# Kernel tuning notes

Measured on AMD Instinct MI355X. Metric: run time of the kernel, lower is better.

The kernel has to match this reference:

```python
import jax, jax.numpy as jnp
import numpy as np

HEADS = 8
DIM_HEAD = 64
SCALE = DIM_HEAD ** -0.5
DIM = 128
HIDDEN = HEADS * DIM_HEAD  # 512


def setup_inputs() -> dict:
    key = jax.random.key(0)
    k1, k2, k3 = jax.random.split(key, 3)
    x = jax.random.normal(k1, (1, DIM, 16, 16, 16), jnp.float32)
    # 1x1x1 Conv3d weights are equivalent to dense (out_ch, in_ch) matrices
    w_qkv = jax.random.normal(k2, (3 * HIDDEN, DIM), jnp.float32) * (DIM ** -0.5)
    w_out = jax.random.normal(k3, (DIM, HIDDEN), jnp.float32) * (HIDDEN ** -0.5)
    b_out = jnp.zeros((DIM,), jnp.float32)
    return {"x": x, "w_qkv": w_qkv, "w_out": w_out, "b_out": b_out}


def reference(x, w_qkv, w_out, b_out):
    b, c, D, H, W = x.shape
    n = D * H * W
    # 1x1x1 conv QKV projection, then split channels as (3, heads, dim_head)
    qkv = jnp.einsum('oc,bcdhw->bodhw', w_qkv, x).reshape(b, 3, HEADS, DIM_HEAD, n)
    q, k, v = qkv[:, 0], qkv[:, 1], qkv[:, 2]  # each (b, h, dim_head, n)
    q = q * SCALE
    # full attention over the flattened 3D volume (n = d*h*w tokens)
    sim = jnp.einsum('bhdi,bhdj->bhij', q, k)           # (b, h, n, n)
    attn = jax.nn.softmax(sim, axis=-1)                 # stable softmax (amax subtracted internally)
    out = jnp.einsum('bhij,bhdj->bhid', attn, v)        # (b, h, n, dim_head)
    out = out.transpose(0, 1, 3, 2).reshape(b, HIDDEN, D, H, W)  # b (h d) x y z
    # 1x1x1 output conv with bias
    out = jnp.einsum('oc,bcdhw->bodhw', w_out, out) + b_out[None, :, None, None, None]
    return out
```

## Files before the change

### kernel.cpp

```cpp
#include <hip/hip_runtime.h>
#include <hip/hip_fp16.h>


#define HEADS 8
#define DHEAD 64
#define NPOS 4096
#define CIN 128
#define HID 512
#define QK_SCALE 0.125f
#define NLOG2E 1.4426950408889634f
#define EXP_BIAS 11.541560327111707f

typedef _Float16 f16;
typedef _Float16 f16x8 __attribute__((ext_vector_type(8)));
typedef _Float16 f16x4 __attribute__((ext_vector_type(4)));
typedef float f32x4 __attribute__((ext_vector_type(4)));

__global__ __launch_bounds__(256) void wconv_kernel(const float* __restrict__ wo,
                                                    f16* __restrict__ woh) {
  int i = (blockIdx.x * 256 + threadIdx.x) * 4;
  f32x4 v = *(const f32x4*)&wo[i];
  f16x4 o = {(f16)v.x, (f16)v.y, (f16)v.z, (f16)v.w};
  *(f16x4*)&woh[i] = o;
}

__global__ __launch_bounds__(256) void qkv_kernel(
    const float* __restrict__ x, const float* __restrict__ w,
    f16* __restrict__ QT, f16* __restrict__ KT, f16* __restrict__ V) {
  __shared__ float xs[64][132];
  __shared__ f16 st[64][72];
  const int bid = blockIdx.x;
  const int ot = bid % 24, pt = bid / 24;
  const int o0 = ot * 64, p0 = pt * 64;
  const int t = threadIdx.x;

  for (int idx = t; idx < 64 * 128; idx += 256) {
    int c = idx >> 6, p = idx & 63;
    xs[p][c] = x[c * NPOS + p0 + p];
  }
  __syncthreads();

  const int pl = (t & 15) * 4;
  const int ol = (t >> 4) * 4;
  float acc[4][4] = {};
  const float* wbase = w + o0 * CIN;
#pragma unroll 4
  for (int c = 0; c < CIN; c += 4) {
    f32x4 xv[4], wv[4];
#pragma unroll
    for (int j = 0; j < 4; ++j) xv[j] = *(const f32x4*)&xs[pl + j][c];
#pragma unroll
    for (int i = 0; i < 4; ++i) wv[i] = *(const f32x4*)&wbase[(ol + i) * CIN + c];
#pragma unroll
    for (int i = 0; i < 4; ++i)
#pragma unroll
      for (int j = 0; j < 4; ++j)
        acc[i][j] += wv[i].x * xv[j].x + wv[i].y * xv[j].y +
                     wv[i].z * xv[j].z + wv[i].w * xv[j].w;
  }

  const int region = o0 >> 9;
  const float scl = (region == 0) ? QK_SCALE : 1.0f;
  if (region < 2) {
#pragma unroll
    for (int i = 0; i < 4; ++i)
#pragma unroll
      for (int j = 0; j < 4; ++j)
        st[pl + j][ol + i] = (f16)(acc[i][j] * scl);
  } else {
#pragma unroll
    for (int i = 0; i < 4; ++i)
#pragma unroll
      for (int j = 0; j < 4; ++j)
        st[ol + i][pl + j] = (f16)acc[i][j];
  }
  __syncthreads();

  const int h = (o0 >> 6) & 7;
  const int row = t >> 2, seg = t & 3;
  const uint4* srcp = (const uint4*)&st[row][seg * 16];
  uint4 v0 = srcp[0], v1 = srcp[1];
  f16* dst;
  if (region == 0)      dst = QT + ((size_t)(h * NPOS + p0 + row)) * DHEAD + seg * 16;
  else if (region == 1) dst = KT + ((size_t)(h * NPOS + p0 + row)) * DHEAD + seg * 16;
  else                  dst = V + ((size_t)(h * DHEAD + row)) * NPOS + p0 + seg * 16;
  ((uint4*)dst)[0] = v0;
  ((uint4*)dst)[1] = v1;
}

__global__ __launch_bounds__(256) void attn_kernel(
    const f16* __restrict__ QT, const f16* __restrict__ KT,
    const f16* __restrict__ V, f16* __restrict__ ATf) {
  __shared__ f16 kbuf[2][4096];
  __shared__ f16 vbuf[2][4096];
  __shared__ f16 plds[4][16][72];
  const int bid = blockIdx.x;
  const int h = bid & 7;
  const int i0 = (bid >> 3) * 64;
  const int t = threadIdx.x;
  const int w = t >> 6, l = t & 63;
  const int g = l >> 4, q = l & 15;
  const int qx = q & 7;

  const f16* kbase = KT + (size_t)h * NPOS * DHEAD;
  const f16* vbase = V + (size_t)h * DHEAD * NPOS;

  const int s0 = w * 128 + l, s1 = s0 + 64;
  const int r0 = s0 >> 3, c0 = (s0 & 7) ^ (r0 & 7);
  const int r1 = s1 >> 3, c1 = (s1 & 7) ^ (r1 & 7);
  const f16* kS0 = kbase + r0 * DHEAD + c0 * 8;
  const f16* kS1 = kbase + r1 * DHEAD + c1 * 8;
  const f16* vS0 = vbase + (size_t)r0 * NPOS + c0 * 8;
  const f16* vS1 = vbase + (size_t)r1 * NPOS + c1 * 8;

#define STAGE(b, j0) do {                                                        \
    __builtin_amdgcn_global_load_lds(                                            \
      (const __attribute__((address_space(1))) unsigned int*)(kS0 + (j0) * DHEAD), \
      (__attribute__((address_space(3))) unsigned int*)(&kbuf[b][w * 1024]), 16, 0, 0); \
    __builtin_amdgcn_global_load_lds(                                            \
      (const __attribute__((address_space(1))) unsigned int*)(kS1 + (j0) * DHEAD), \
      (__attribute__((address_space(3))) unsigned int*)(&kbuf[b][w * 1024 + 512]), 16, 0, 0); \
    __builtin_amdgcn_global_load_lds(                                            \
      (const __attribute__((address_space(1))) unsigned int*)(vS0 + (j0)),       \
      (__attribute__((address_space(3))) unsigned int*)(&vbuf[b][w * 1024]), 16, 0, 0); \
    __builtin_amdgcn_global_load_lds(                                            \
      (const __attribute__((address_space(1))) unsigned int*)(vS1 + (j0)),       \
      (__attribute__((address_space(3))) unsigned int*)(&vbuf[b][w * 1024 + 512]), 16, 0, 0); \
  } while (0)

  STAGE(0, 0);

  const f16* qbase = QT + ((size_t)(h * NPOS + i0 + 16 * w + q)) * DHEAD + 8 * g;
  const f16x8 qa0 = *(const f16x8*)(qbase);
  const f16x8 qa1 = *(const f16x8*)(qbase + 32);

  f32x4 O[4] = {};
  float lsum[4] = {};
  const int kof0 = q * 128 + ((g ^ qx) << 4);
  const int kof1 = q * 128 + (((g + 4) ^ qx) << 4);

  __syncthreads();
  int cur = 0;
  for (int jt = 0; jt < 64; ++jt) {
    if (jt + 1 < 64) STAGE(cur ^ 1, (jt + 1) * 64);
    const char* kb = (const char*)kbuf[cur];
    const char* vbp = (const char*)vbuf[cur];
    f32x4 S[4];
#pragma unroll
    for (int js = 0; js < 4; ++js) {
      f16x8 kb0 = *(const f16x8*)(kb + js * 2048 + kof0);
      f16x8 kb1 = *(const f16x8*)(kb + js * 2048 + kof1);
      f32x4 z = {};
      z = __builtin_amdgcn_mfma_f32_16x16x32_f16(qa0, kb0, z, 0, 0, 0);
      z = __builtin_amdgcn_mfma_f32_16x16x32_f16(qa1, kb1, z, 0, 0, 0);
      S[js] = z;
    }
#pragma unroll
    for (int js = 0; js < 4; ++js) {
#pragma unroll
      for (int r = 0; r < 4; ++r) {
        float p = exp2f(__builtin_fmaf(S[js][r], NLOG2E, -EXP_BIAS));
        lsum[r] += p;
        plds[w][4 * g + r][16 * js + q] = (f16)p;
      }
    }
#pragma unroll
    for (int ks = 0; ks < 2; ++ks) {
      f16x8 pa = *(const f16x8*)&plds[w][q][32 * ks + 8 * g];
      const int vof = q * 128 + (((4 * ks + g) ^ qx) << 4);
#pragma unroll
      for (int td = 0; td < 4; ++td) {
        f16x8 vv = *(const f16x8*)(vbp + td * 2048 + vof);
        O[td] = __builtin_amdgcn_mfma_f32_16x16x32_f16(pa, vv, O[td], 0, 0, 0);
      }
    }
    __syncthreads();
    cur ^= 1;
  }
#undef STAGE

#pragma unroll
  for (int r = 0; r < 4; ++r) {
    float s = lsum[r];
#pragma unroll
    for (int off = 1; off < 16; off <<= 1) s += __shfl_xor(s, off, 16);
    lsum[r] = 1.0f / s;
  }
#pragma unroll
  for (int td = 0; td < 4; ++td)
#pragma unroll
    for (int r = 0; r < 4; ++r) {
      int row = i0 + 16 * w + 4 * g + r;
      ATf[(size_t)row * HID + h * DHEAD + 16 * td + q] = (f16)(O[td][r] * lsum[r]);
    }
}

__global__ __launch_bounds__(256) void out_kernel(
    const f16* __restrict__ ATf, const f16* __restrict__ woh,
    const float* __restrict__ bo, float* __restrict__ out) {
  const int bid = blockIdx.x;
  const int o0 = (bid >> 6) * 32;
  const int p0 = (bid & 63) * 64;
  const int t = threadIdx.x;
  const int w = t >> 6, l = t & 63;
  const int g = l >> 4, q = l & 15;
  const int oa = o0 + 16 * (w >> 1);
  const int pa = p0 + 32 * (w & 1);
  f32x4 acc[2] = {};
  const f16* arow0 = ATf + (size_t)(pa + q) * HID + 8 * g;
  const f16* arow1 = ATf + (size_t)(pa + 16 + q) * HID + 8 * g;
  const f16* wrow = woh + (size_t)(oa + q) * HID + 8 * g;
#pragma unroll 4
  for (int k0 = 0; k0 < HID; k0 += 32) {
    f16x8 a = *(const f16x8*)(wrow + k0);
    f16x8 b0 = *(const f16x8*)(arow0 + k0);
    f16x8 b1 = *(const f16x8*)(arow1 + k0);
    acc[0] = __builtin_amdgcn_mfma_f32_16x16x32_f16(a, b0, acc[0], 0, 0, 0);
    acc[1] = __builtin_amdgcn_mfma_f32_16x16x32_f16(a, b1, acc[1], 0, 0, 0);
  }
#pragma unroll
  for (int s = 0; s < 2; ++s)
#pragma unroll
    for (int r = 0; r < 4; ++r) {
      int o = oa + 4 * g + r;
      out[(size_t)o * NPOS + pa + 16 * s + q] = acc[s][r] + bo[o];
    }
}

extern "C" void kernel_launch(void* const* d_in, const int* in_sizes, int n_in,
                              void* d_out, int out_size, void* d_ws, size_t ws_size,
                              hipStream_t stream) {
  const float* x    = (const float*)d_in[0];
  const float* wqkv = (const float*)d_in[1];
  const float* wout = (const float*)d_in[2];
  const float* bout = (const float*)d_in[3];
  float* out = (float*)d_out;
  char* ws = (char*)d_ws;
  f16* QT  = (f16*)(ws);
  f16* KT  = (f16*)(ws + (4u << 20));
  f16* V   = (f16*)(ws + (8u << 20));
  f16* ATf = (f16*)(ws + (12u << 20));
  f16* woh = (f16*)(ws + (16u << 20));

  wconv_kernel<<<64, 256, 0, stream>>>(wout, woh);
  qkv_kernel<<<1536, 256, 0, stream>>>(x, wqkv, QT, KT, V);
  attn_kernel<<<512, 256, 0, stream>>>(QT, KT, V, ATf);
  out_kernel<<<256, 256, 0, stream>>>(ATf, woh, bout, out);
}
```

Baseline: 201.9 us.

## Split attention keys across waves, move QKV projection to fp16 MFMA

The QKV projection now pre-converts x and the weights to fp16 (with the softmax scale and log2e folded into the Q weights) and runs on MFMA instead of scalar fp32 FMAs. The attention kernel takes 32 query rows per block and splits the key range across the four waves. Each wave loads K and V straight from global memory with no LDS staging or barriers, and the partial outputs and sums are combined through shared memory at the end. The aim is more blocks in flight and less per-tile synchronisation, at the cost of unshared global K/V loads, extra conversion launches, and an fp16 rounding of the scaled Q weights.

```diff
diff --git a/kernel.cpp b/kernel.cpp
--- a/kernel.cpp
+++ b/kernel.cpp
@@ -7,14 +7,15 @@
 #define NPOS 4096
 #define CIN 128
 #define HID 512
-#define QK_SCALE 0.125f
-#define NLOG2E 1.4426950408889634f
+#define SC_Q 0.18033688011116953f
 #define EXP_BIAS 11.541560327111707f
 
 typedef _Float16 f16;
 typedef _Float16 f16x8 __attribute__((ext_vector_type(8)));
 typedef _Float16 f16x4 __attribute__((ext_vector_type(4)));
 typedef float f32x4 __attribute__((ext_vector_type(4)));
+
+#define MFMA16(a, b, c) __builtin_amdgcn_mfma_f32_16x16x32_f16(a, b, c, 0, 0, 0)
 
 __global__ __launch_bounds__(256) void wconv_kernel(const float* __restrict__ wo,
                                                     f16* __restrict__ woh) {
@@ -24,175 +25,194 @@
   *(f16x4*)&woh[i] = o;
 }
 
-__global__ __launch_bounds__(256) void qkv_kernel(
-    const float* __restrict__ x, const float* __restrict__ w,
+__global__ __launch_bounds__(256) void wqkvconv_kernel(const float* __restrict__ w,
+                                                       f16* __restrict__ wh) {
+  int i = (blockIdx.x * 256 + threadIdx.x) * 4;
+  const int o = i >> 7;
+  const float scl = (o < 512) ? SC_Q : 1.0f;
+  f32x4 v = *(const f32x4*)&w[i];
+  f16x4 r = {(f16)(v.x * scl), (f16)(v.y * scl), (f16)(v.z * scl), (f16)(v.w * scl)};
+  *(f16x4*)&wh[i] = r;
+}
+
+__global__ __launch_bounds__(256) void xconv_kernel(const float* __restrict__ x,
+                                                    f16* __restrict__ xh) {
+  __shared__ f16 xt[32][136];
+  const int p0 = blockIdx.x * 32;
+  const int t = threadIdx.x;
+  for (int i = t; i < 32 * 128; i += 256) {
+    int c = i >> 5, p = i & 31;
+    xt[p][c] = (f16)x[c * NPOS + p0 + p];
+  }
+  __syncthreads();
+  const int p = t >> 3, cs = (t & 7) * 16;
+  f16x8 a = *(const f16x8*)&xt[p][cs];
+  f16x8 b = *(const f16x8*)&xt[p][cs + 8];
+  *(f16x8*)(xh + (size_t)(p0 + p) * CIN + cs) = a;
+  *(f16x8*)(xh + (size_t)(p0 + p) * CIN + cs + 8) = b;
+}
+
+__global__ __launch_bounds__(256) void qkvg_kernel(
+    const f16* __restrict__ wh, const f16* __restrict__ xh,
     f16* __restrict__ QT, f16* __restrict__ KT, f16* __restrict__ V) {
-  __shared__ float xs[64][132];
-  __shared__ f16 st[64][72];
   const int bid = blockIdx.x;
-  const int ot = bid % 24, pt = bid / 24;
-  const int o0 = ot * 64, p0 = pt * 64;
-  const int t = threadIdx.x;
-
-  for (int idx = t; idx < 64 * 128; idx += 256) {
-    int c = idx >> 6, p = idx & 63;
-    xs[p][c] = x[c * NPOS + p0 + p];
-  }
-  __syncthreads();
-
-  const int pl = (t & 15) * 4;
-  const int ol = (t >> 4) * 4;
-  float acc[4][4] = {};
-  const float* wbase = w + o0 * CIN;
-#pragma unroll 4
-  for (int c = 0; c < CIN; c += 4) {
-    f32x4 xv[4], wv[4];
-#pragma unroll
-    for (int j = 0; j < 4; ++j) xv[j] = *(const f32x4*)&xs[pl + j][c];
-#pragma unroll
-    for (int i = 0; i < 4; ++i) wv[i] = *(const f32x4*)&wbase[(ol + i) * CIN + c];
-#pragma unroll
-    for (int i = 0; i < 4; ++i)
-#pragma unroll
-      for (int j = 0; j < 4; ++j)
-        acc[i][j] += wv[i].x * xv[j].x + wv[i].y * xv[j].y +
-                     wv[i].z * xv[j].z + wv[i].w * xv[j].w;
-  }
-
-  const int region = o0 >> 9;
-  const float scl = (region == 0) ? QK_SCALE : 1.0f;
-  if (region < 2) {
-#pragma unroll
-    for (int i = 0; i < 4; ++i)
-#pragma unroll
-      for (int j = 0; j < 4; ++j)
-        st[pl + j][ol + i] = (f16)(acc[i][j] * scl);
+  const int o0 = (bid % 24) * 64, pa = (bid / 24) * 64;
+  const int t = threadIdx.x;
+  const int wo = t >> 6, l = t & 63;
+  const int g = l >> 4, q = l & 15;
+  const int oa = o0 + 16 * wo;
+  const f16* wrow = wh + (size_t)(oa + q) * CIN + 8 * g;
+  f32x4 acc[4] = {};
+  if (o0 < 1024) {
+#pragma unroll
+    for (int kt = 0; kt < 4; ++kt) {
+      f16x8 a = *(const f16x8*)(wrow + 32 * kt);
+#pragma unroll
+      for (int pj = 0; pj < 4; ++pj) {
+        f16x8 b = *(const f16x8*)(xh + (size_t)(pa + 16 * pj + q) * CIN + 32 * kt + 8 * g);
+        acc[pj] = MFMA16(a, b, acc[pj]);
+      }
+    }
+    f16* dst = (o0 < 512) ? QT : KT;
+    const int hh = (oa >> 6) & 7;
+    const int d0 = (oa & 63) + 4 * g;
+#pragma unroll
+    for (int pj = 0; pj < 4; ++pj) {
+      f16x4 o4 = {(f16)acc[pj][0], (f16)acc[pj][1], (f16)acc[pj][2], (f16)acc[pj][3]};
+      *(f16x4*)(dst + ((size_t)(hh * NPOS + pa + 16 * pj + q)) * DHEAD + d0) = o4;
+    }
   } else {
 #pragma unroll
-    for (int i = 0; i < 4; ++i)
-#pragma unroll
-      for (int j = 0; j < 4; ++j)
-        st[ol + i][pl + j] = (f16)acc[i][j];
-  }
-  __syncthreads();
-
-  const int h = (o0 >> 6) & 7;
-  const int row = t >> 2, seg = t & 3;
-  const uint4* srcp = (const uint4*)&st[row][seg * 16];
-  uint4 v0 = srcp[0], v1 = srcp[1];
-  f16* dst;
-  if (region == 0)      dst = QT + ((size_t)(h * NPOS + p0 + row)) * DHEAD + seg * 16;
-  else if (region == 1) dst = KT + ((size_t)(h * NPOS + p0 + row)) * DHEAD + seg * 16;
-  else                  dst = V + ((size_t)(h * DHEAD + row)) * NPOS + p0 + seg * 16;
-  ((uint4*)dst)[0] = v0;
-  ((uint4*)dst)[1] = v1;
-}
-
-__global__ __launch_bounds__(256) void attn_kernel(
+    for (int kt = 0; kt < 4; ++kt) {
+      f16x8 b = *(const f16x8*)(wrow + 32 * kt);
+#pragma unroll
+      for (int pj = 0; pj < 4; ++pj) {
+        f16x8 a = *(const f16x8*)(xh + (size_t)(pa + 16 * pj + q) * CIN + 32 * kt + 8 * g);
+        acc[pj] = MFMA16(a, b, acc[pj]);
+      }
+    }
+    const int hv = oa - 1024;
+    const int hh = hv >> 6;
+    const int d = (hv & 63) + q;
+#pragma unroll
+    for (int pj = 0; pj < 4; ++pj) {
+      f16x4 o4 = {(f16)acc[pj][0], (f16)acc[pj][1], (f16)acc[pj][2], (f16)acc[pj][3]};
+      *(f16x4*)(V + ((size_t)(hh * DHEAD + d)) * NPOS + pa + 16 * pj + 4 * g) = o4;
+    }
+  }
+}
+
+__global__ __launch_bounds__(256, 4) void attn_kernel(
     const f16* __restrict__ QT, const f16* __restrict__ KT,
     const f16* __restrict__ V, f16* __restrict__ ATf) {
-  __shared__ f16 kbuf[2][4096];
-  __shared__ f16 vbuf[2][4096];
-  __shared__ f16 plds[4][16][72];
+  __shared__ float comb[3][32][65];
+  __shared__ float lcomb[3][32];
+  __shared__ f16 plds[4][32][36];
   const int bid = blockIdx.x;
   const int h = bid & 7;
-  const int i0 = (bid >> 3) * 64;
+  const int i0 = (bid >> 3) * 32;
   const int t = threadIdx.x;
   const int w = t >> 6, l = t & 63;
   const int g = l >> 4, q = l & 15;
-  const int qx = q & 7;
 
   const f16* kbase = KT + (size_t)h * NPOS * DHEAD;
   const f16* vbase = V + (size_t)h * DHEAD * NPOS;
 
-  const int s0 = w * 128 + l, s1 = s0 + 64;
-  const int r0 = s0 >> 3, c0 = (s0 & 7) ^ (r0 & 7);
-  const int r1 = s1 >> 3, c1 = (s1 & 7) ^ (r1 & 7);
-  const f16* kS0 = kbase + r0 * DHEAD + c0 * 8;
-  const f16* kS1 = kbase + r1 * DHEAD + c1 * 8;
-  const f16* vS0 = vbase + (size_t)r0 * NPOS + c0 * 8;
-  const f16* vS1 = vbase + (size_t)r1 * NPOS + c1 * 8;
-
-#define STAGE(b, j0) do {                                                        \
-    __builtin_amdgcn_global_load_lds(                                            \
-      (const __attribute__((address_space(1))) unsigned int*)(kS0 + (j0) * DHEAD), \
-      (__attribute__((address_space(3))) unsigned int*)(&kbuf[b][w * 1024]), 16, 0, 0); \
-    __builtin_amdgcn_global_load_lds(                                            \
-      (const __attribute__((address_space(1))) unsigned int*)(kS1 + (j0) * DHEAD), \
-      (__attribute__((address_space(3))) unsigned int*)(&kbuf[b][w * 1024 + 512]), 16, 0, 0); \
-    __builtin_amdgcn_global_load_lds(                                            \
-      (const __attribute__((address_space(1))) unsigned int*)(vS0 + (j0)),       \
-      (__attribute__((address_space(3))) unsigned int*)(&vbuf[b][w * 1024]), 16, 0, 0); \
-    __builtin_amdgcn_global_load_lds(                                            \
-      (const __attribute__((address_space(1))) unsigned int*)(vS1 + (j0)),       \
-      (__attribute__((address_space(3))) unsigned int*)(&vbuf[b][w * 1024 + 512]), 16, 0, 0); \
-  } while (0)
-
-  STAGE(0, 0);
-
-  const f16* qbase = QT + ((size_t)(h * NPOS + i0 + 16 * w + q)) * DHEAD + 8 * g;
-  const f16x8 qa0 = *(const f16x8*)(qbase);
-  const f16x8 qa1 = *(const f16x8*)(qbase + 32);
-
-  f32x4 O[4] = {};
-  float lsum[4] = {};
-  const int kof0 = q * 128 + ((g ^ qx) << 4);
-  const int kof1 = q * 128 + (((g + 4) ^ qx) << 4);
-
+  f16x8 qa[2][2];
+#pragma unroll
+  for (int rs = 0; rs < 2; ++rs) {
+    const f16* qp = QT + ((size_t)(h * NPOS + i0 + 16 * rs + q)) * DHEAD + 8 * g;
+    qa[rs][0] = *(const f16x8*)qp;
+    qa[rs][1] = *(const f16x8*)(qp + 32);
+  }
+
+  f32x4 O[2][4] = {};
+  float lsum[2][4] = {};
+  const f32x4 zinit = {-EXP_BIAS, -EXP_BIAS, -EXP_BIAS, -EXP_BIAS};
+
+  for (int jt = 0; jt < 32; ++jt) {
+    const int j0 = w * 1024 + jt * 32;
+    f16x8 kb[2][2], vv[4];
+#pragma unroll
+    for (int js = 0; js < 2; ++js) {
+      const f16* kp = kbase + (size_t)(j0 + 16 * js + q) * DHEAD + 8 * g;
+      kb[js][0] = *(const f16x8*)kp;
+      kb[js][1] = *(const f16x8*)(kp + 32);
+    }
+#pragma unroll
+    for (int td = 0; td < 4; ++td)
+      vv[td] = *(const f16x8*)(vbase + (size_t)(16 * td + q) * NPOS + j0 + 8 * g);
+
+#pragma unroll
+    for (int rs = 0; rs < 2; ++rs)
+#pragma unroll
+      for (int js = 0; js < 2; ++js) {
+        f32x4 z = zinit;
+        z = MFMA16(qa[rs][0], kb[js][0], z);
+        z = MFMA16(qa[rs][1], kb[js][1], z);
+#pragma unroll
+        for (int r = 0; r < 4; ++r) {
+          float p = exp2f(z[r]);
+          lsum[rs][r] += p;
+          plds[w][16 * rs + 4 * g + r][16 * js + q] = (f16)p;
+        }
+      }
+#pragma unroll
+    for (int rs = 0; rs < 2; ++rs) {
+      f16x8 pa = *(const f16x8*)&plds[w][16 * rs + q][8 * g];
+#pragma unroll
+      for (int td = 0; td < 4; ++td)
+        O[rs][td] = MFMA16(pa, vv[td], O[rs][td]);
+    }
+  }
+
+#pragma unroll
+  for (int rs = 0; rs < 2; ++rs)
+#pragma unroll
+    for (int r = 0; r < 4; ++r) {
+      float s = lsum[rs][r];
+#pragma unroll
+      for (int off = 1; off < 16; off <<= 1) s += __shfl_xor(s, off, 16);
+      lsum[rs][r] = s;
+    }
+
+  if (w > 0) {
+#pragma unroll
+    for (int rs = 0; rs < 2; ++rs)
+#pragma unroll
+      for (int td = 0; td < 4; ++td)
+#pragma unroll
+        for (int r = 0; r < 4; ++r)
+          comb[w - 1][16 * rs + 4 * g + r][16 * td + q] = O[rs][td][r];
+    if (q == 0)
+#pragma unroll
+      for (int rs = 0; rs < 2; ++rs)
+#pragma unroll
+        for (int r = 0; r < 4; ++r)
+          lcomb[w - 1][16 * rs + 4 * g + r] = lsum[rs][r];
+  }
   __syncthreads();
-  int cur = 0;
-  for (int jt = 0; jt < 64; ++jt) {
-    if (jt + 1 < 64) STAGE(cur ^ 1, (jt + 1) * 64);
-    const char* kb = (const char*)kbuf[cur];
-    const char* vbp = (const char*)vbuf[cur];
-    f32x4 S[4];
-#pragma unroll
-    for (int js = 0; js < 4; ++js) {
-      f16x8 kb0 = *(const f16x8*)(kb + js * 2048 + kof0);
-      f16x8 kb1 = *(const f16x8*)(kb + js * 2048 + kof1);
-      f32x4 z = {};
-      z = __builtin_amdgcn_mfma_f32_16x16x32_f16(qa0, kb0, z, 0, 0, 0);
-      z = __builtin_amdgcn_mfma_f32_16x16x32_f16(qa1, kb1, z, 0, 0, 0);
-      S[js] = z;
-    }
-#pragma unroll
-    for (int js = 0; js < 4; ++js) {
+  if (w == 0) {
+#pragma unroll
+    for (int rs = 0; rs < 2; ++rs) {
+      float linv[4];
 #pragma unroll
       for (int r = 0; r < 4; ++r) {
-        float p = exp2f(__builtin_fmaf(S[js][r], NLOG2E, -EXP_BIAS));
-        lsum[r] += p;
-        plds[w][4 * g + r][16 * js + q] = (f16)p;
-      }
-    }
-#pragma unroll
-    for (int ks = 0; ks < 2; ++ks) {
-      f16x8 pa = *(const f16x8*)&plds[w][q][32 * ks + 8 * g];
-      const int vof = q * 128 + (((4 * ks + g) ^ qx) << 4);
-#pragma unroll
-      for (int td = 0; td < 4; ++td) {
-        f16x8 vv = *(const f16x8*)(vbp + td * 2048 + vof);
-        O[td] = __builtin_amdgcn_mfma_f32_16x16x32_f16(pa, vv, O[td], 0, 0, 0);
-      }
-    }
-    __syncthreads();
-    cur ^= 1;
-  }
-#undef STAGE
-
-#pragma unroll
-  for (int r = 0; r < 4; ++r) {
-    float s = lsum[r];
-#pragma unroll
-    for (int off = 1; off < 16; off <<= 1) s += __shfl_xor(s, off, 16);
-    lsum[r] = 1.0f / s;
-  }
-#pragma unroll
-  for (int td = 0; td < 4; ++td)
-#pragma unroll
-    for (int r = 0; r < 4; ++r) {
-      int row = i0 + 16 * w + 4 * g + r;
-      ATf[(size_t)row * HID + h * DHEAD + 16 * td + q] = (f16)(O[td][r] * lsum[r]);
-    }
+        int row = 16 * rs + 4 * g + r;
+        float s = lsum[rs][r] + lcomb[0][row] + lcomb[1][row] + lcomb[2][row];
+        linv[r] = 1.0f / s;
+      }
+#pragma unroll
+      for (int td = 0; td < 4; ++td)
+#pragma unroll
+        for (int r = 0; r < 4; ++r) {
+          int row = 16 * rs + 4 * g + r;
+          float v = O[rs][td][r] + comb[0][row][16 * td + q] +
+                    comb[1][row][16 * td + q] + comb[2][row][16 * td + q];
+          ATf[(size_t)(i0 + row) * HID + h * DHEAD + 16 * td + q] = (f16)(v * linv[r]);
+        }
+    }
+  }
 }
 
 __global__ __launch_bounds__(256) void out_kernel(
@@ -215,8 +235,8 @@
     f16x8 a = *(const f16x8*)(wrow + k0);
     f16x8 b0 = *(const f16x8*)(arow0 + k0);
     f16x8 b1 = *(const f16x8*)(arow1 + k0);
-    acc[0] = __builtin_amdgcn_mfma_f32_16x16x32_f16(a, b0, acc[0], 0, 0, 0);
-    acc[1] = __builtin_amdgcn_mfma_f32_16x16x32_f16(a, b1, acc[1], 0, 0, 0);
+    acc[0] = MFMA16(a, b0, acc[0]);
+    acc[1] = MFMA16(a, b1, acc[1]);
   }
 #pragma unroll
   for (int s = 0; s < 2; ++s)
@@ -241,9 +261,13 @@
   f16* V   = (f16*)(ws + (8u << 20));
   f16* ATf = (f16*)(ws + (12u << 20));
   f16* woh = (f16*)(ws + (16u << 20));
+  f16* wqh = (f16*)(ws + (16u << 20) + (128u << 10));
+  f16* xh  = (f16*)(ws + (16u << 20) + (512u << 10));
 
   wconv_kernel<<<64, 256, 0, stream>>>(wout, woh);
-  qkv_kernel<<<1536, 256, 0, stream>>>(x, wqkv, QT, KT, V);
-  attn_kernel<<<512, 256, 0, stream>>>(QT, KT, V, ATf);
+  wqkvconv_kernel<<<192, 256, 0, stream>>>(wqkv, wqh);
+  xconv_kernel<<<128, 256, 0, stream>>>(x, xh);
+  qkvg_kernel<<<1536, 256, 0, stream>>>(wqh, xh, QT, KT, V);
+  attn_kernel<<<1024, 256, 0, stream>>>(QT, KT, V, ATf);
   out_kernel<<<256, 256, 0, stream>>>(ATf, woh, bout, out);
 }
```

New measurement: 217.4 us. 1.08x slower.
